# Kernel tuning notes

Hardware: AMD Instinct MI355X
Metric: run time of the kernel (lower is better)

The kernel has to match this reference:

```python
import jax, jax.numpy as jnp
import numpy as np

RANGE_DISP = 32
IND_INPUT_VIEW = np.array([1, 9]) - 1  # 0-based indices of the two input views
TOTAL_VIEWS = 9                         # an_sparse + an_novel
FEAT_CH = 64


def conv2d(x, w, b):
    # x: (N, Cin, H, W), w: (Cout, Cin, kh, kw), SAME padding, stride 1
    y = jax.lax.conv_general_dilated(x, w, (1, 1), 'SAME',
                                     dimension_numbers=('NCHW', 'OIHW', 'NCHW'))
    return y + b[None, :, None, None]


def unfold_1xK(x, K):
    # torch.nn.functional.unfold(x, kernel_size=(1, K)) for x: (M, C, H, W)
    # -> (M, C, K, H*(W-K+1)), column index = h*(W-K+1) + w (row-major).
    M, C, H, W = x.shape
    out_w = W - K + 1
    cols = jnp.arange(out_w)[None, :] + jnp.arange(K)[:, None]  # (K, out_w)
    y = x[:, :, :, cols]             # (M, C, H, K, out_w)
    y = y.transpose(0, 1, 3, 2, 4)   # (M, C, K, H, out_w)
    return y.reshape(M, C, K, H * out_w)


def setup_inputs() -> dict:
    key = jax.random.key(0)
    ks = jax.random.split(key, 24)
    b, an_sparse, an_novel, rp = 2, 2, 7, 32
    K = RANGE_DISP
    ps = rp + K - 1  # 63

    def rn(k, shape, s=1.0):
        return jax.random.normal(k, shape, dtype=jnp.float32) * s

    W = 0.05  # weight init scale
    return {
        'lf_sparse':        rn(ks[0], (b, an_sparse, rp, ps)),
        'flow_sparse':      rn(ks[1], (b, an_sparse, rp, ps)),
        'warped_lf_sparse': rn(ks[2], (b, an_sparse, rp, ps)),
        'patch_left':       rn(ks[3], (b, an_novel, rp, rp)),
        'patch_right':      rn(ks[4], (b, an_novel, rp, rp)),
        # FlowRefNet: 3 -> 64 -> 64 -> 64, 3x3 convs, SAME
        'fr_w1': rn(ks[5], (FEAT_CH, 3, 3, 3), W), 'fr_b1': jnp.zeros((FEAT_CH,), jnp.float32),
        'fr_w2': rn(ks[6], (FEAT_CH, FEAT_CH, 3, 3), W), 'fr_b2': jnp.zeros((FEAT_CH,), jnp.float32),
        'fr_w3': rn(ks[7], (FEAT_CH, FEAT_CH, 3, 3), W), 'fr_b3': jnp.zeros((FEAT_CH,), jnp.float32),
        # MlpNet: per-disparity MLP 67 -> 64 -> 64 -> 1 (weight head) + conf head 64 -> 1
        'mlp_w1': rn(ks[8], (67, 64), W), 'mlp_b1': jnp.zeros((64,), jnp.float32),
        'mlp_w2': rn(ks[9], (64, 64), W), 'mlp_b2': jnp.zeros((64,), jnp.float32),
        'mlp_w3': rn(ks[10], (64, 1), W), 'mlp_b3': jnp.zeros((1,), jnp.float32),
        'conf_w': rn(ks[11], (64, 1), W), 'conf_b': jnp.zeros((1,), jnp.float32),
        # ViewRefNet: 3 -> 64 -> 64 -> 1 convs, residual on novel patch
        'vr_w1': rn(ks[12], (FEAT_CH, 3, 3, 3), W), 'vr_b1': jnp.zeros((FEAT_CH,), jnp.float32),
        'vr_w2': rn(ks[13], (FEAT_CH, FEAT_CH, 3, 3), W), 'vr_b2': jnp.zeros((FEAT_CH,), jnp.float32),
        'vr_w3': rn(ks[14], (1, FEAT_CH, 3, 3), W), 'vr_b3': jnp.zeros((1,), jnp.float32),
    }


def reference(lf_sparse, flow_sparse, warped_lf_sparse, patch_left, patch_right,
              fr_w1, fr_b1, fr_w2, fr_b2, fr_w3, fr_b3,
              mlp_w1, mlp_b1, mlp_w2, mlp_b2, mlp_w3, mlp_b3, conf_w, conf_b,
              vr_w1, vr_b1, vr_w2, vr_b2, vr_w3, vr_b3):
    b, an_sparse, rp, ps = lf_sparse.shape
    an_novel = patch_left.shape[1]
    K = RANGE_DISP
    N = rp * rp

    lf = lf_sparse.reshape(b * an_sparse, 1, rp, ps)
    fl = flow_sparse.reshape(b * an_sparse, 1, rp, ps)
    wp = warped_lf_sparse.reshape(b * an_sparse, 1, rp, ps)

    # FlowRefNet: flow-feature extraction
    h = jax.nn.relu(conv2d(jnp.concatenate([fl, lf, wp], axis=1), fr_w1, fr_b1))
    h = jax.nn.relu(conv2d(h, fr_w2, fr_b2))
    feat = jax.nn.relu(conv2d(h, fr_w3, fr_b3))  # (b*as, 64, rp, ps)

    # angular code: input-view index minus novel-view index
    ind_novel = np.delete(np.arange(TOTAL_VIEWS), IND_INPUT_VIEW)
    ang = jnp.asarray(IND_INPUT_VIEW[None, :] - ind_novel[:, None], dtype=lf.dtype)  # (an, as)
    spatial = (jnp.arange(K) - K // 2).astype(lf.dtype)  # (K,)

    # EPI windows via unfold(kernel=(1, K))
    flow_unf = unfold_1xK(fl, K)[:, 0]  # (b*as, K, N)
    feat_unf = unfold_1xK(feat, K)      # (b*as, 64, K, N)

    sh = (b, an_novel, an_sparse)
    f_flow = jnp.broadcast_to(flow_unf.reshape(b, 1, an_sparse, 1, K, N),  sh + (1, K, N))
    f_feat = jnp.broadcast_to(feat_unf.reshape(b, 1, an_sparse, FEAT_CH, K, N), sh + (FEAT_CH, K, N))
    f_spat = jnp.broadcast_to(spatial.reshape(1, 1, 1, 1, K, 1),           sh + (1, K, N))
    f_ang  = jnp.broadcast_to(ang.reshape(1, an_novel, an_sparse, 1, 1, 1), sh + (1, K, N))
    features = jnp.concatenate([f_flow, f_feat, f_spat, f_ang], axis=3)  # (b, an, as, 67, K, N)
    # -> (b*an*as*N, K, 67) matching permute(0,3,2,1).reshape in torch
    features = features.transpose(0, 1, 2, 5, 4, 3).reshape(-1, K, 67)

    # MlpNet: per-disparity weight + per-sample confidence
    h1 = jax.nn.relu(features @ mlp_w1 + mlp_b1)
    h2 = jax.nn.relu(h1 @ mlp_w2 + mlp_b2)          # (M2, K, 64)
    weight = (h2 @ mlp_w3 + mlp_b3)[..., 0]         # (M2, K)
    conf = (h2.mean(axis=1) @ conf_w + conf_b)[..., 0]  # (M2,)

    weight = jax.nn.softmax(weight.reshape(b, an_novel, an_sparse, N, K), axis=-1)
    confs = jax.nn.softmax(conf.reshape(b, an_novel, an_sparse, N), axis=2)

    # disparity-weighted combination over EPI windows
    epi = unfold_1xK(lf, K)[:, 0].reshape(b, an_sparse, K, N)
    nv = jnp.einsum('bskn,bvsnk->bvsn', epi, weight)   # (b, an, as, N)
    novel = (nv * confs).sum(axis=2)                   # (b, an, N)

    # ViewRefNet: residual refinement
    pn = novel.reshape(b * an_novel, 1, rp, rp)
    pl = patch_left.reshape(b * an_novel, 1, rp, rp)
    pr = patch_right.reshape(b * an_novel, 1, rp, rp)
    g = jax.nn.relu(conv2d(jnp.concatenate([pn, pl, pr], axis=1), vr_w1, vr_b1))
    g = jax.nn.relu(conv2d(g, vr_w2, vr_b2))
    res = conv2d(g, vr_w3, vr_b3)
    out = pn + res
    return out.reshape(b, an_novel, rp, rp)
```

## Files before the change

kernel.cpp:

```cpp
#include <hip/hip_runtime.h>

typedef unsigned short u16;
typedef unsigned int u32;
typedef __bf16 bf16x8 __attribute__((ext_vector_type(8)));
typedef float f32x4 __attribute__((ext_vector_type(4)));
typedef u16 u16x8 __attribute__((ext_vector_type(8)));

__device__ __forceinline__ u16 f2bf(float f) {
    __bf16 h = (__bf16)f;
    return __builtin_bit_cast(u16, h);
}
__device__ __forceinline__ float bf2f(u16 u) {
    unsigned int x = ((unsigned int)u) << 16;
    return __builtin_bit_cast(float, x);
}

union FragU { u16x8 u; bf16x8 v; };

constexpr size_t X1     = 0;
constexpr size_t X2     = 258048;
constexpr size_t FEATBF = 516096;
constexpr size_t NVOFF  = 774144;
constexpr size_t CFOFF  = 802816;
constexpr size_t NOVEL  = 831488;
constexpr size_t Y1     = 845824;
constexpr size_t Y2     = 1304576;

template<int W, int NPX>
__global__ __launch_bounds__(256) void conv1_kernel(
    const float* __restrict__ in0, const float* __restrict__ in1,
    const float* __restrict__ in2,
    const float* __restrict__ wts, const float* __restrict__ bias,
    u16* __restrict__ out)
{
    constexpr int H = 32;
    const int t = threadIdx.x;
    const int px = blockIdx.y * 256 + t;
    const int m = blockIdx.z;
    const int og = blockIdx.x;
    if (px >= NPX) return;
    const int y = px / W, x = px - y * W;

    float acc[8];
#pragma unroll
    for (int oc = 0; oc < 8; ++oc) acc[oc] = bias[og * 8 + oc];

#pragma unroll
    for (int cin = 0; cin < 3; ++cin) {
        const float* ip = (cin == 0 ? in0 : (cin == 1 ? in1 : in2)) + (size_t)m * NPX;
        float tap[9];
#pragma unroll
        for (int dy = 0; dy < 3; ++dy) {
            int yy = y + dy - 1;
            bool ry = (yy >= 0) && (yy < H);
#pragma unroll
            for (int dx = 0; dx < 3; ++dx) {
                int xx = x + dx - 1;
                tap[dy * 3 + dx] = (ry && xx >= 0 && xx < W) ? ip[yy * W + xx] : 0.f;
            }
        }
#pragma unroll
        for (int oc = 0; oc < 8; ++oc) {
            const float* wr = wts + (size_t)(og * 8 + oc) * 27 + cin * 9;
#pragma unroll
            for (int j = 0; j < 9; ++j) acc[oc] = fmaf(tap[j], wr[j], acc[oc]);
        }
    }
    u16x8 pk;
#pragma unroll
    for (int oc = 0; oc < 8; ++oc) pk[oc] = f2bf(fmaxf(acc[oc], 0.f));
    *(u16x8*)(out + ((size_t)m * NPX + px) * 64 + og * 8) = pk;
}

template<int W, int NPX>
__global__ __launch_bounds__(256) void convmfma_kernel(
    const u16* __restrict__ in, const float* __restrict__ wts,
    const float* __restrict__ bias, u16* __restrict__ out)
{
    constexpr int H = 32;
    __shared__ u16 sw[5 * 64 * 64];

    const int t = threadIdx.x;
    const int base = blockIdx.x * 64;
    const int m = blockIdx.y;
    const int w = t >> 6, lane = t & 63, q = lane >> 4, l15 = lane & 15;

    const u16* im = in + (size_t)m * NPX * 64;
    const int pxA = base + w * 16 + l15;
    const int yA = pxA / W, xA = pxA - yA * W;
    const bool pxok = (pxA < NPX);

    f32x4 acc[4];
#pragma unroll
    for (int nt = 0; nt < 4; ++nt) acc[nt] = f32x4{0.f, 0.f, 0.f, 0.f};

#pragma unroll
    for (int phase = 0; phase < 2; ++phase) {
        const int tp0 = phase * 5;
        const int ntap = phase ? 4 : 5;
        if (phase) __syncthreads();
        for (int i = t; i < ntap * 4096; i += 256) {
            int tap = tp0 + (i >> 12), och = (i >> 6) & 63, cin = i & 63;
            sw[i] = f2bf(wts[(size_t)och * 576 + cin * 9 + tap]);
        }
        __syncthreads();
#pragma unroll
        for (int tl = 0; tl < 5; ++tl) {
            if (tl >= ntap) break;
            const int tap = tp0 + tl;
            const int dy = tap / 3 - 1, dx = tap % 3 - 1;
            const bool valid = pxok && (yA + dy >= 0) && (yA + dy < H)
                                    && (xA + dx >= 0) && (xA + dx < W);
            const u16* ap = im + (size_t)(pxA + dy * W + dx) * 64;
            FragU a0, a1;
            if (valid) {
                a0 = *(const FragU*)(ap + q * 8);
                a1 = *(const FragU*)(ap + 32 + q * 8);
            } else {
#pragma unroll
                for (int jj = 0; jj < 8; ++jj) { a0.u[jj] = 0; a1.u[jj] = 0; }
            }
#pragma unroll
            for (int nt = 0; nt < 4; ++nt) {
                const u16* bp = sw + tl * 4096 + (nt * 16 + l15) * 64;
                FragU b0 = *(const FragU*)(bp + q * 8);
                FragU b1 = *(const FragU*)(bp + 32 + q * 8);
                acc[nt] = __builtin_amdgcn_mfma_f32_16x16x32_bf16(a0.v, b0.v, acc[nt], 0, 0, 0);
                acc[nt] = __builtin_amdgcn_mfma_f32_16x16x32_bf16(a1.v, b1.v, acc[nt], 0, 0, 0);
            }
        }
    }

#pragma unroll
    for (int nt = 0; nt < 4; ++nt) {
        const float bb = bias[nt * 16 + l15];
#pragma unroll
        for (int e = 0; e < 4; ++e) {
            int pxs = base + w * 16 + q * 4 + e;
            if (pxs < NPX)
                out[((size_t)m * NPX + pxs) * 64 + nt * 16 + l15] =
                    f2bf(fmaxf(acc[nt][e] + bb, 0.f));
        }
    }
}

__global__ __launch_bounds__(256, 2) void mlp_mfma_kernel(
    const float* __restrict__ lf, const float* __restrict__ flow,
    const u16* __restrict__ feat,
    const float* __restrict__ w1, const float* __restrict__ b1,
    const float* __restrict__ w2, const float* __restrict__ b2,
    const float* __restrict__ w3, const float* __restrict__ b3g,
    const float* __restrict__ cw, const float* __restrict__ cbg,
    float* __restrict__ nv_out, float* __restrict__ cf_out)
{
    constexpr int SBS = 72;
    __shared__ u16 s_w1[67 * 64];
    __shared__ u16 s_w2[64 * 64];
    __shared__ __align__(16) float s_vec[7 * 64];
    __shared__ __align__(16) float s_flow[256];
    __shared__ __align__(16) float s_epi[256];
    __shared__ __align__(16) u16 s_base[256 * SBS];

    const int t = threadIdx.x;
    const int blk = blockIdx.x;
    const int bs = blk >> 7;
    const int n0 = (blk & 127) * 8;
    const int b = bs >> 1, s = bs & 1;
    const int w = t >> 6, lane = t & 63, q = lane >> 4, l15 = lane & 15;

    for (int i = t; i < 67 * 64; i += 256) s_w1[i] = f2bf(w1[i]);
    for (int i = t; i < 64 * 64; i += 256) s_w2[i] = f2bf(w2[i]);
    if (t < 64) {
        s_vec[t]       = b1[t];
        s_vec[64 + t]  = b2[t];
        s_vec[128 + t] = w3[t];
        s_vec[192 + t] = cw[t];
        s_vec[256 + t] = w1[t];
        s_vec[320 + t] = w1[65 * 64 + t];
        s_vec[384 + t] = w1[66 * 64 + t];
    }
    {
        int nl = t >> 5, k = t & 31;
        int n = n0 + nl;
        int a = (bs * 32 + (n >> 5)) * 63 + (n & 31) + k;
        s_flow[t] = flow[a];
        s_epi[t]  = lf[a];
    }
    __syncthreads();

    const float b3s = b3g[0];
    const float cbs = cbg[0];

    FragU w1b[2][4];
#pragma unroll
    for (int ks = 0; ks < 2; ++ks)
#pragma unroll
        for (int nt = 0; nt < 4; ++nt)
#pragma unroll
            for (int jj = 0; jj < 8; ++jj)
                w1b[ks][nt].u[jj] = s_w1[(1 + ks * 32 + q * 8 + jj) * 64 + nt * 16 + l15];

    float w1r0pl[4], w1r65pl[4], b1pl[4];
#pragma unroll
    for (int nt = 0; nt < 4; ++nt) {
        int j1 = nt * 16 + l15;
        w1r0pl[nt]  = s_vec[256 + j1];
        w1r65pl[nt] = s_vec[320 + j1];
        b1pl[nt]    = s_vec[j1];
    }

#pragma unroll
    for (int mt = 0; mt < 4; ++mt) {
        const int rbase = w * 64 + mt * 16;
        FragU af[2];
        {
            int r = rbase + l15;
            int n = n0 + (r >> 5);
            int pos = (n >> 5) * 63 + (n & 31) + (r & 31);
            const u16* fp = feat + ((size_t)bs * 2016 + pos) * 64;
            af[0] = *(const FragU*)(fp + q * 8);
            af[1] = *(const FragU*)(fp + 32 + q * 8);
        }
        f32x4 flow4 = *(const f32x4*)(s_flow + rbase + q * 4);
#pragma unroll
        for (int nt = 0; nt < 4; ++nt) {
            f32x4 d = {0.f, 0.f, 0.f, 0.f};
            d = __builtin_amdgcn_mfma_f32_16x16x32_bf16(af[0].v, w1b[0][nt].v, d, 0, 0, 0);
            d = __builtin_amdgcn_mfma_f32_16x16x32_bf16(af[1].v, w1b[1][nt].v, d, 0, 0, 0);
#pragma unroll
            for (int e = 0; e < 4; ++e) {
                int r = rbase + q * 4 + e;
                int k = r & 31;
                float val = d[e] + flow4[e] * w1r0pl[nt]
                          + (float)(k - 16) * w1r65pl[nt] + b1pl[nt];
                s_base[r * SBS + nt * 16 + l15] = f2bf(val);
            }
        }
    }
    __syncthreads();

    FragU w2a[4][2];
#pragma unroll
    for (int mt = 0; mt < 4; ++mt)
#pragma unroll
        for (int ks = 0; ks < 2; ++ks)
#pragma unroll
            for (int jj = 0; jj < 8; ++jj)
                w2a[mt][ks].u[jj] = s_w2[(ks * 32 + q * 8 + jj) * 64 + mt * 16 + l15];

    float w66pl[2][8];
#pragma unroll
    for (int ks = 0; ks < 2; ++ks)
#pragma unroll
        for (int jj = 0; jj < 8; ++jj)
            w66pl[ks][jj] = s_vec[384 + ks * 32 + q * 8 + jj];

    float b2pl[4][4], w3pl[4][4], cwpl[4][4];
#pragma unroll
    for (int mt = 0; mt < 4; ++mt)
#pragma unroll
        for (int e = 0; e < 4; ++e) {
            b2pl[mt][e] = s_vec[64 + mt * 16 + q * 4 + e];
            w3pl[mt][e] = s_vec[128 + mt * 16 + q * 4 + e];
            cwpl[mt][e] = s_vec[192 + mt * 16 + q * 4 + e];
        }
    float epi_pl[4];
#pragma unroll
    for (int nt = 0; nt < 4; ++nt) epi_pl[nt] = s_epi[w * 64 + nt * 16 + l15];

    for (int v = 0; v < 7; ++v) {
        float ang = (s == 0) ? -(float)(v + 1) : (float)(7 - v);
        f32x4 acc[4][4];
#pragma unroll
        for (int nt = 0; nt < 4; ++nt) {
            FragU bfr[2];
#pragma unroll
            for (int ks = 0; ks < 2; ++ks) {
                const u16x8 raw = *(const u16x8*)(s_base + (w * 64 + nt * 16 + l15) * SBS + ks * 32 + q * 8);
#pragma unroll
                for (int jj = 0; jj < 8; ++jj) {
                    float xv = bf2f(raw[jj]);
                    float hv = fmaxf(xv + ang * w66pl[ks][jj], 0.f);
                    bfr[ks].u[jj] = f2bf(hv);
                }
            }
#pragma unroll
            for (int mt = 0; mt < 4; ++mt) {
                f32x4 d = {0.f, 0.f, 0.f, 0.f};
                d = __builtin_amdgcn_mfma_f32_16x16x32_bf16(w2a[mt][0].v, bfr[0].v, d, 0, 0, 0);
                d = __builtin_amdgcn_mfma_f32_16x16x32_bf16(w2a[mt][1].v, bfr[1].v, d, 0, 0, 0);
                acc[mt][nt] = d;
            }
        }
        float wl[4], cfl[4];
#pragma unroll
        for (int nt = 0; nt < 4; ++nt) {
            float wls = 0.f, cfs = 0.f;
#pragma unroll
            for (int mt = 0; mt < 4; ++mt)
#pragma unroll
                for (int e = 0; e < 4; ++e) {
                    float h2 = fmaxf(acc[mt][nt][e] + b2pl[mt][e], 0.f);
                    wls += h2 * w3pl[mt][e];
                    cfs += h2 * cwpl[mt][e];
                }
            wls += __shfl_xor(wls, 16); wls += __shfl_xor(wls, 32);
            cfs += __shfl_xor(cfs, 16); cfs += __shfl_xor(cfs, 32);
            wl[nt]  = wls + b3s;
            cfl[nt] = cfs;
        }
#pragma unroll
        for (int ni = 0; ni < 2; ++ni) {
            float a0 = wl[ni * 2], a1 = wl[ni * 2 + 1];
            float mx = fmaxf(a0, a1);
#pragma unroll
            for (int msk = 1; msk <= 8; msk <<= 1) mx = fmaxf(mx, __shfl_xor(mx, msk));
            float e0 = __expf(a0 - mx), e1 = __expf(a1 - mx);
            float ssum = e0 + e1;
            float nvp = e0 * epi_pl[ni * 2] + e1 * epi_pl[ni * 2 + 1];
            float cfp = cfl[ni * 2] + cfl[ni * 2 + 1];
#pragma unroll
            for (int msk = 1; msk <= 8; msk <<= 1) {
                ssum += __shfl_xor(ssum, msk);
                nvp  += __shfl_xor(nvp, msk);
                cfp  += __shfl_xor(cfp, msk);
            }
            if (lane == 0) {
                int n = n0 + w * 2 + ni;
                size_t idx = ((size_t)(b * 7 + v) * 2 + s) * 1024 + n;
                nv_out[idx] = nvp / ssum;
                cf_out[idx] = cfp * (1.f / 32.f) + cbs;
            }
        }
    }
}

__global__ void combine_kernel(const float* __restrict__ nv, const float* __restrict__ cf,
                               float* __restrict__ novel) {
    int tid = blockIdx.x * 256 + threadIdx.x;
    if (tid >= 2 * 7 * 1024) return;
    int n = tid & 1023;
    int bv = tid >> 10;
    size_t i0 = ((size_t)bv * 2 + 0) * 1024 + n;
    size_t i1 = ((size_t)bv * 2 + 1) * 1024 + n;
    float c0 = cf[i0], c1 = cf[i1];
    float mx = fmaxf(c0, c1);
    float e0 = __expf(c0 - mx), e1 = __expf(c1 - mx);
    novel[tid] = (e0 * nv[i0] + e1 * nv[i1]) / (e0 + e1);
}

__global__ __launch_bounds__(256) void convlast_kernel(
    const u16* __restrict__ in,
    const float* __restrict__ wts,
    const float* __restrict__ bias,
    const float* __restrict__ resid,
    float* __restrict__ out)
{
    __shared__ float sw3[576];
    const int t = threadIdx.x;
    for (int i = t; i < 576; i += 256) sw3[i] = wts[i];
    __syncthreads();

    const int tid = blockIdx.x * 256 + t;
    const int m = tid >> 10, p = tid & 1023;
    const int y = p >> 5, x = p & 31;
    float a = bias[0] + resid[tid];
    const u16* im = in + ((size_t)m * 1024 + p) * 64;
#pragma unroll
    for (int dy = 0; dy < 3; ++dy) {
        int yy = y + dy - 1;
        if (yy < 0 || yy >= 32) continue;
#pragma unroll
        for (int dx = 0; dx < 3; ++dx) {
            int xx = x + dx - 1;
            if (xx < 0 || xx >= 32) continue;
            const u16* ip = im + (size_t)((dy - 1) * 32 + (dx - 1)) * 64;
            const int tap = dy * 3 + dx;
#pragma unroll
            for (int cg = 0; cg < 8; ++cg) {
                u16x8 raw = *(const u16x8*)(ip + cg * 8);
#pragma unroll
                for (int e = 0; e < 8; ++e)
                    a = fmaf(bf2f(raw[e]), sw3[(cg * 8 + e) * 9 + tap], a);
            }
        }
    }
    out[tid] = a;
}

extern "C" void kernel_launch(void* const* d_in, const int* in_sizes, int n_in,
                              void* d_out, int out_size, void* d_ws, size_t ws_size,
                              hipStream_t stream) {
    const float* lf   = (const float*)d_in[0];
    const float* flow = (const float*)d_in[1];
    const float* wp   = (const float*)d_in[2];
    const float* pl   = (const float*)d_in[3];
    const float* pr   = (const float*)d_in[4];
    float* ws = (float*)d_ws;

    conv1_kernel<63, 2016><<<dim3(8, 8, 4), 256, 0, stream>>>(
        flow, lf, wp, (const float*)d_in[5], (const float*)d_in[6],
        (u16*)(ws + X1));
    convmfma_kernel<63, 2016><<<dim3(32, 4), 256, 0, stream>>>(
        (const u16*)(ws + X1), (const float*)d_in[7], (const float*)d_in[8],
        (u16*)(ws + X2));
    convmfma_kernel<63, 2016><<<dim3(32, 4), 256, 0, stream>>>(
        (const u16*)(ws + X2), (const float*)d_in[9], (const float*)d_in[10],
        (u16*)(ws + FEATBF));

    mlp_mfma_kernel<<<512, 256, 0, stream>>>(
        lf, flow, (const u16*)(ws + FEATBF),
        (const float*)d_in[11], (const float*)d_in[12],
        (const float*)d_in[13], (const float*)d_in[14],
        (const float*)d_in[15], (const float*)d_in[16],
        (const float*)d_in[17], (const float*)d_in[18],
        ws + NVOFF, ws + CFOFF);

    combine_kernel<<<56, 256, 0, stream>>>(ws + NVOFF, ws + CFOFF, ws + NOVEL);

    conv1_kernel<32, 1024><<<dim3(8, 4, 14), 256, 0, stream>>>(
        ws + NOVEL, pl, pr, (const float*)d_in[19], (const float*)d_in[20],
        (u16*)(ws + Y1));
    convmfma_kernel<32, 1024><<<dim3(16, 14), 256, 0, stream>>>(
        (const u16*)(ws + Y1), (const float*)d_in[21], (const float*)d_in[22],
        (u16*)(ws + Y2));
    convlast_kernel<<<56, 256, 0, stream>>>(
        (const u16*)(ws + Y2), (const float*)d_in[23], (const float*)d_in[24],
        ws + NOVEL, (float*)d_out);
}
```

Measured before the change: 201.3 us.

## Precompute bf16 weights once, read MFMA fragments from global, fuse combine into MLP

Adds a prep kernel that converts and reorders the conv and MLP weights to bf16 once per call, so the conv and MLP kernels no longer stage and convert weights in shared memory with extra barriers. The conv kernels now load B fragments directly from global/L2. The MLP kernel is restructured so each block handles both sparse views for a batch and loops over two groups of four samples, allowing the confidence softmax combine to happen in shared memory and removing the separate combine kernel. It adds one launch and halves the MLP grid, which may lower parallelism.

```diff
diff --git a/kernel.cpp b/kernel.cpp
--- a/kernel.cpp
+++ b/kernel.cpp
@@ -17,14 +17,40 @@
 
 union FragU { u16x8 u; bf16x8 v; };
 
-constexpr size_t X1     = 0;
-constexpr size_t X2     = 258048;
-constexpr size_t FEATBF = 516096;
-constexpr size_t NVOFF  = 774144;
-constexpr size_t CFOFF  = 802816;
-constexpr size_t NOVEL  = 831488;
-constexpr size_t Y1     = 845824;
-constexpr size_t Y2     = 1304576;
+constexpr size_t WB2F  = 0;
+constexpr size_t WB3F  = 18432;
+constexpr size_t WBV2  = 36864;
+constexpr size_t W1T   = 55296;
+constexpr size_t W2T   = 57344;
+constexpr size_t X1    = 59392;
+constexpr size_t X2    = 317440;
+constexpr size_t FEATBF= 575488;
+constexpr size_t NOVEL = 833536;
+constexpr size_t Y1    = 847872;
+constexpr size_t Y2    = 1306624;
+
+__global__ __launch_bounds__(256) void prep_kernel(
+    const float* __restrict__ frw2, const float* __restrict__ frw3,
+    const float* __restrict__ vrw2,
+    const float* __restrict__ mw1, const float* __restrict__ mw2,
+    u16* __restrict__ wb2, u16* __restrict__ wb3, u16* __restrict__ wbv,
+    u16* __restrict__ w1t, u16* __restrict__ w2t)
+{
+    const int tid = blockIdx.x * 256 + threadIdx.x;
+    const int stride = gridDim.x * 256;
+    for (int i = tid; i < 36864; i += stride) {
+        int tap = i >> 12, och = (i >> 6) & 63, cin = i & 63;
+        size_t s = (size_t)och * 576 + cin * 9 + tap;
+        wb2[i] = f2bf(frw2[s]);
+        wb3[i] = f2bf(frw3[s]);
+        wbv[i] = f2bf(vrw2[s]);
+    }
+    for (int i = tid; i < 4096; i += stride) {
+        int col = i >> 6, r = i & 63;
+        w1t[i] = f2bf(mw1[(1 + r) * 64 + col]);
+        w2t[i] = f2bf(mw2[r * 64 + col]);
+    }
+}
 
 template<int W, int NPX>
 __global__ __launch_bounds__(256) void conv1_kernel(
@@ -74,12 +100,10 @@
 
 template<int W, int NPX>
 __global__ __launch_bounds__(256) void convmfma_kernel(
-    const u16* __restrict__ in, const float* __restrict__ wts,
+    const u16* __restrict__ in, const u16* __restrict__ wbf,
     const float* __restrict__ bias, u16* __restrict__ out)
 {
     constexpr int H = 32;
-    __shared__ u16 sw[5 * 64 * 64];
-
     const int t = threadIdx.x;
     const int base = blockIdx.x * 64;
     const int m = blockIdx.y;
@@ -95,39 +119,26 @@
     for (int nt = 0; nt < 4; ++nt) acc[nt] = f32x4{0.f, 0.f, 0.f, 0.f};
 
 #pragma unroll
-    for (int phase = 0; phase < 2; ++phase) {
-        const int tp0 = phase * 5;
-        const int ntap = phase ? 4 : 5;
-        if (phase) __syncthreads();
-        for (int i = t; i < ntap * 4096; i += 256) {
-            int tap = tp0 + (i >> 12), och = (i >> 6) & 63, cin = i & 63;
-            sw[i] = f2bf(wts[(size_t)och * 576 + cin * 9 + tap]);
-        }
-        __syncthreads();
-#pragma unroll
-        for (int tl = 0; tl < 5; ++tl) {
-            if (tl >= ntap) break;
-            const int tap = tp0 + tl;
-            const int dy = tap / 3 - 1, dx = tap % 3 - 1;
-            const bool valid = pxok && (yA + dy >= 0) && (yA + dy < H)
-                                    && (xA + dx >= 0) && (xA + dx < W);
-            const u16* ap = im + (size_t)(pxA + dy * W + dx) * 64;
-            FragU a0, a1;
-            if (valid) {
-                a0 = *(const FragU*)(ap + q * 8);
-                a1 = *(const FragU*)(ap + 32 + q * 8);
-            } else {
-#pragma unroll
-                for (int jj = 0; jj < 8; ++jj) { a0.u[jj] = 0; a1.u[jj] = 0; }
-            }
-#pragma unroll
-            for (int nt = 0; nt < 4; ++nt) {
-                const u16* bp = sw + tl * 4096 + (nt * 16 + l15) * 64;
-                FragU b0 = *(const FragU*)(bp + q * 8);
-                FragU b1 = *(const FragU*)(bp + 32 + q * 8);
-                acc[nt] = __builtin_amdgcn_mfma_f32_16x16x32_bf16(a0.v, b0.v, acc[nt], 0, 0, 0);
-                acc[nt] = __builtin_amdgcn_mfma_f32_16x16x32_bf16(a1.v, b1.v, acc[nt], 0, 0, 0);
-            }
+    for (int tap = 0; tap < 9; ++tap) {
+        const int dy = tap / 3 - 1, dx = tap % 3 - 1;
+        const bool valid = pxok && (yA + dy >= 0) && (yA + dy < H)
+                                && (xA + dx >= 0) && (xA + dx < W);
+        const u16* ap = im + (size_t)(pxA + dy * W + dx) * 64;
+        FragU a0, a1;
+        if (valid) {
+            a0 = *(const FragU*)(ap + q * 8);
+            a1 = *(const FragU*)(ap + 32 + q * 8);
+        } else {
+#pragma unroll
+            for (int jj = 0; jj < 8; ++jj) { a0.u[jj] = 0; a1.u[jj] = 0; }
+        }
+#pragma unroll
+        for (int nt = 0; nt < 4; ++nt) {
+            const u16* bp = wbf + tap * 4096 + (nt * 16 + l15) * 64;
+            FragU b0 = *(const FragU*)(bp + q * 8);
+            FragU b1 = *(const FragU*)(bp + 32 + q * 8);
+            acc[nt] = __builtin_amdgcn_mfma_f32_16x16x32_bf16(a0.v, b0.v, acc[nt], 0, 0, 0);
+            acc[nt] = __builtin_amdgcn_mfma_f32_16x16x32_bf16(a1.v, b1.v, acc[nt], 0, 0, 0);
         }
     }
 
@@ -147,29 +158,29 @@
 __global__ __launch_bounds__(256, 2) void mlp_mfma_kernel(
     const float* __restrict__ lf, const float* __restrict__ flow,
     const u16* __restrict__ feat,
+    const u16* __restrict__ w1t, const u16* __restrict__ w2t,
     const float* __restrict__ w1, const float* __restrict__ b1,
-    const float* __restrict__ w2, const float* __restrict__ b2,
+    const float* __restrict__ b2,
     const float* __restrict__ w3, const float* __restrict__ b3g,
     const float* __restrict__ cw, const float* __restrict__ cbg,
-    float* __restrict__ nv_out, float* __restrict__ cf_out)
+    float* __restrict__ novel)
 {
     constexpr int SBS = 72;
-    __shared__ u16 s_w1[67 * 64];
-    __shared__ u16 s_w2[64 * 64];
     __shared__ __align__(16) float s_vec[7 * 64];
     __shared__ __align__(16) float s_flow[256];
     __shared__ __align__(16) float s_epi[256];
     __shared__ __align__(16) u16 s_base[256 * SBS];
+    __shared__ float s_nv[2][7][4];
+    __shared__ float s_cf[2][7][4];
 
     const int t = threadIdx.x;
     const int blk = blockIdx.x;
-    const int bs = blk >> 7;
-    const int n0 = (blk & 127) * 8;
-    const int b = bs >> 1, s = bs & 1;
+    const int b = blk >> 7;
+    const int n0base = (blk & 127) * 8;
     const int w = t >> 6, lane = t & 63, q = lane >> 4, l15 = lane & 15;
-
-    for (int i = t; i < 67 * 64; i += 256) s_w1[i] = f2bf(w1[i]);
-    for (int i = t; i < 64 * 64; i += 256) s_w2[i] = f2bf(w2[i]);
+    const int sw = w >> 1;
+    const int bsw = b * 2 + sw;
+
     if (t < 64) {
         s_vec[t]       = b1[t];
         s_vec[64 + t]  = b2[t];
@@ -179,13 +190,6 @@
         s_vec[320 + t] = w1[65 * 64 + t];
         s_vec[384 + t] = w1[66 * 64 + t];
     }
-    {
-        int nl = t >> 5, k = t & 31;
-        int n = n0 + nl;
-        int a = (bs * 32 + (n >> 5)) * 63 + (n & 31) + k;
-        s_flow[t] = flow[a];
-        s_epi[t]  = lf[a];
-    }
     __syncthreads();
 
     const float b3s = b3g[0];
@@ -196,9 +200,14 @@
     for (int ks = 0; ks < 2; ++ks)
 #pragma unroll
         for (int nt = 0; nt < 4; ++nt)
-#pragma unroll
-            for (int jj = 0; jj < 8; ++jj)
-                w1b[ks][nt].u[jj] = s_w1[(1 + ks * 32 + q * 8 + jj) * 64 + nt * 16 + l15];
+            w1b[ks][nt] = *(const FragU*)(w1t + (nt * 16 + l15) * 64 + ks * 32 + q * 8);
+
+    FragU w2a[4][2];
+#pragma unroll
+    for (int mt = 0; mt < 4; ++mt)
+#pragma unroll
+        for (int ks = 0; ks < 2; ++ks)
+            w2a[mt][ks] = *(const FragU*)(w2t + (mt * 16 + l15) * 64 + ks * 32 + q * 8);
 
     float w1r0pl[4], w1r65pl[4], b1pl[4];
 #pragma unroll
@@ -208,53 +217,12 @@
         w1r65pl[nt] = s_vec[320 + j1];
         b1pl[nt]    = s_vec[j1];
     }
-
-#pragma unroll
-    for (int mt = 0; mt < 4; ++mt) {
-        const int rbase = w * 64 + mt * 16;
-        FragU af[2];
-        {
-            int r = rbase + l15;
-            int n = n0 + (r >> 5);
-            int pos = (n >> 5) * 63 + (n & 31) + (r & 31);
-            const u16* fp = feat + ((size_t)bs * 2016 + pos) * 64;
-            af[0] = *(const FragU*)(fp + q * 8);
-            af[1] = *(const FragU*)(fp + 32 + q * 8);
-        }
-        f32x4 flow4 = *(const f32x4*)(s_flow + rbase + q * 4);
-#pragma unroll
-        for (int nt = 0; nt < 4; ++nt) {
-            f32x4 d = {0.f, 0.f, 0.f, 0.f};
-            d = __builtin_amdgcn_mfma_f32_16x16x32_bf16(af[0].v, w1b[0][nt].v, d, 0, 0, 0);
-            d = __builtin_amdgcn_mfma_f32_16x16x32_bf16(af[1].v, w1b[1][nt].v, d, 0, 0, 0);
-#pragma unroll
-            for (int e = 0; e < 4; ++e) {
-                int r = rbase + q * 4 + e;
-                int k = r & 31;
-                float val = d[e] + flow4[e] * w1r0pl[nt]
-                          + (float)(k - 16) * w1r65pl[nt] + b1pl[nt];
-                s_base[r * SBS + nt * 16 + l15] = f2bf(val);
-            }
-        }
-    }
-    __syncthreads();
-
-    FragU w2a[4][2];
-#pragma unroll
-    for (int mt = 0; mt < 4; ++mt)
-#pragma unroll
-        for (int ks = 0; ks < 2; ++ks)
-#pragma unroll
-            for (int jj = 0; jj < 8; ++jj)
-                w2a[mt][ks].u[jj] = s_w2[(ks * 32 + q * 8 + jj) * 64 + mt * 16 + l15];
-
     float w66pl[2][8];
 #pragma unroll
     for (int ks = 0; ks < 2; ++ks)
 #pragma unroll
         for (int jj = 0; jj < 8; ++jj)
             w66pl[ks][jj] = s_vec[384 + ks * 32 + q * 8 + jj];
-
     float b2pl[4][4], w3pl[4][4], cwpl[4][4];
 #pragma unroll
     for (int mt = 0; mt < 4; ++mt)
@@ -264,89 +232,128 @@
             w3pl[mt][e] = s_vec[128 + mt * 16 + q * 4 + e];
             cwpl[mt][e] = s_vec[192 + mt * 16 + q * 4 + e];
         }
-    float epi_pl[4];
-#pragma unroll
-    for (int nt = 0; nt < 4; ++nt) epi_pl[nt] = s_epi[w * 64 + nt * 16 + l15];
-
-    for (int v = 0; v < 7; ++v) {
-        float ang = (s == 0) ? -(float)(v + 1) : (float)(7 - v);
-        f32x4 acc[4][4];
-#pragma unroll
-        for (int nt = 0; nt < 4; ++nt) {
-            FragU bfr[2];
-#pragma unroll
-            for (int ks = 0; ks < 2; ++ks) {
-                const u16x8 raw = *(const u16x8*)(s_base + (w * 64 + nt * 16 + l15) * SBS + ks * 32 + q * 8);
-#pragma unroll
-                for (int jj = 0; jj < 8; ++jj) {
-                    float xv = bf2f(raw[jj]);
-                    float hv = fmaxf(xv + ang * w66pl[ks][jj], 0.f);
-                    bfr[ks].u[jj] = f2bf(hv);
+
+#pragma unroll 1
+    for (int iter = 0; iter < 2; ++iter) {
+        const int n0 = n0base + iter * 4;
+        {
+            int ss = t >> 7, nl = (t >> 5) & 3, k = t & 31;
+            int n = n0 + nl;
+            int a = ((b * 2 + ss) * 32 + (n >> 5)) * 63 + (n & 31) + k;
+            s_flow[t] = flow[a];
+            s_epi[t]  = lf[a];
+        }
+        __syncthreads();
+
+#pragma unroll
+        for (int mt = 0; mt < 4; ++mt) {
+            const int rbase = w * 64 + mt * 16;
+            FragU af[2];
+            {
+                int r = rbase + l15;
+                int n = n0 + ((r >> 5) & 3);
+                int pos = (n >> 5) * 63 + (n & 31) + (r & 31);
+                const u16* fp = feat + ((size_t)bsw * 2016 + pos) * 64;
+                af[0] = *(const FragU*)(fp + q * 8);
+                af[1] = *(const FragU*)(fp + 32 + q * 8);
+            }
+            f32x4 flow4 = *(const f32x4*)(s_flow + rbase + q * 4);
+#pragma unroll
+            for (int nt = 0; nt < 4; ++nt) {
+                f32x4 d = {0.f, 0.f, 0.f, 0.f};
+                d = __builtin_amdgcn_mfma_f32_16x16x32_bf16(af[0].v, w1b[0][nt].v, d, 0, 0, 0);
+                d = __builtin_amdgcn_mfma_f32_16x16x32_bf16(af[1].v, w1b[1][nt].v, d, 0, 0, 0);
+#pragma unroll
+                for (int e = 0; e < 4; ++e) {
+                    int r = rbase + q * 4 + e;
+                    int k = r & 31;
+                    float val = d[e] + flow4[e] * w1r0pl[nt]
+                              + (float)(k - 16) * w1r65pl[nt] + b1pl[nt];
+                    s_base[r * SBS + nt * 16 + l15] = f2bf(val);
                 }
             }
-#pragma unroll
-            for (int mt = 0; mt < 4; ++mt) {
-                f32x4 d = {0.f, 0.f, 0.f, 0.f};
-                d = __builtin_amdgcn_mfma_f32_16x16x32_bf16(w2a[mt][0].v, bfr[0].v, d, 0, 0, 0);
-                d = __builtin_amdgcn_mfma_f32_16x16x32_bf16(w2a[mt][1].v, bfr[1].v, d, 0, 0, 0);
-                acc[mt][nt] = d;
-            }
-        }
-        float wl[4], cfl[4];
-#pragma unroll
-        for (int nt = 0; nt < 4; ++nt) {
-            float wls = 0.f, cfs = 0.f;
-#pragma unroll
-            for (int mt = 0; mt < 4; ++mt)
-#pragma unroll
-                for (int e = 0; e < 4; ++e) {
-                    float h2 = fmaxf(acc[mt][nt][e] + b2pl[mt][e], 0.f);
-                    wls += h2 * w3pl[mt][e];
-                    cfs += h2 * cwpl[mt][e];
+        }
+        __syncthreads();
+
+        float epi_pl[4];
+#pragma unroll
+        for (int nt = 0; nt < 4; ++nt) epi_pl[nt] = s_epi[w * 64 + nt * 16 + l15];
+
+        for (int v = 0; v < 7; ++v) {
+            float ang = (sw == 0) ? -(float)(v + 1) : (float)(7 - v);
+            f32x4 acc[4][4];
+#pragma unroll
+            for (int nt = 0; nt < 4; ++nt) {
+                FragU bfr[2];
+#pragma unroll
+                for (int ks = 0; ks < 2; ++ks) {
+                    const u16x8 raw = *(const u16x8*)(s_base + (w * 64 + nt * 16 + l15) * SBS + ks * 32 + q * 8);
+#pragma unroll
+                    for (int jj = 0; jj < 8; ++jj) {
+                        float xv = bf2f(raw[jj]);
+                        float hv = fmaxf(xv + ang * w66pl[ks][jj], 0.f);
+                        bfr[ks].u[jj] = f2bf(hv);
+                    }
                 }
-            wls += __shfl_xor(wls, 16); wls += __shfl_xor(wls, 32);
-            cfs += __shfl_xor(cfs, 16); cfs += __shfl_xor(cfs, 32);
-            wl[nt]  = wls + b3s;
-            cfl[nt] = cfs;
-        }
-#pragma unroll
-        for (int ni = 0; ni < 2; ++ni) {
-            float a0 = wl[ni * 2], a1 = wl[ni * 2 + 1];
-            float mx = fmaxf(a0, a1);
-#pragma unroll
-            for (int msk = 1; msk <= 8; msk <<= 1) mx = fmaxf(mx, __shfl_xor(mx, msk));
-            float e0 = __expf(a0 - mx), e1 = __expf(a1 - mx);
-            float ssum = e0 + e1;
-            float nvp = e0 * epi_pl[ni * 2] + e1 * epi_pl[ni * 2 + 1];
-            float cfp = cfl[ni * 2] + cfl[ni * 2 + 1];
-#pragma unroll
-            for (int msk = 1; msk <= 8; msk <<= 1) {
-                ssum += __shfl_xor(ssum, msk);
-                nvp  += __shfl_xor(nvp, msk);
-                cfp  += __shfl_xor(cfp, msk);
-            }
-            if (lane == 0) {
-                int n = n0 + w * 2 + ni;
-                size_t idx = ((size_t)(b * 7 + v) * 2 + s) * 1024 + n;
-                nv_out[idx] = nvp / ssum;
-                cf_out[idx] = cfp * (1.f / 32.f) + cbs;
-            }
-        }
-    }
-}
-
-__global__ void combine_kernel(const float* __restrict__ nv, const float* __restrict__ cf,
-                               float* __restrict__ novel) {
-    int tid = blockIdx.x * 256 + threadIdx.x;
-    if (tid >= 2 * 7 * 1024) return;
-    int n = tid & 1023;
-    int bv = tid >> 10;
-    size_t i0 = ((size_t)bv * 2 + 0) * 1024 + n;
-    size_t i1 = ((size_t)bv * 2 + 1) * 1024 + n;
-    float c0 = cf[i0], c1 = cf[i1];
-    float mx = fmaxf(c0, c1);
-    float e0 = __expf(c0 - mx), e1 = __expf(c1 - mx);
-    novel[tid] = (e0 * nv[i0] + e1 * nv[i1]) / (e0 + e1);
+#pragma unroll
+                for (int mt = 0; mt < 4; ++mt) {
+                    f32x4 d = {0.f, 0.f, 0.f, 0.f};
+                    d = __builtin_amdgcn_mfma_f32_16x16x32_bf16(w2a[mt][0].v, bfr[0].v, d, 0, 0, 0);
+                    d = __builtin_amdgcn_mfma_f32_16x16x32_bf16(w2a[mt][1].v, bfr[1].v, d, 0, 0, 0);
+                    acc[mt][nt] = d;
+                }
+            }
+            float wl[4], cfl[4];
+#pragma unroll
+            for (int nt = 0; nt < 4; ++nt) {
+                float wls = 0.f, cfs = 0.f;
+#pragma unroll
+                for (int mt = 0; mt < 4; ++mt)
+#pragma unroll
+                    for (int e = 0; e < 4; ++e) {
+                        float h2 = fmaxf(acc[mt][nt][e] + b2pl[mt][e], 0.f);
+                        wls += h2 * w3pl[mt][e];
+                        cfs += h2 * cwpl[mt][e];
+                    }
+                wls += __shfl_xor(wls, 16); wls += __shfl_xor(wls, 32);
+                cfs += __shfl_xor(cfs, 16); cfs += __shfl_xor(cfs, 32);
+                wl[nt]  = wls + b3s;
+                cfl[nt] = cfs;
+            }
+#pragma unroll
+            for (int ni = 0; ni < 2; ++ni) {
+                float a0 = wl[ni * 2], a1 = wl[ni * 2 + 1];
+                float mx = fmaxf(a0, a1);
+#pragma unroll
+                for (int msk = 1; msk <= 8; msk <<= 1) mx = fmaxf(mx, __shfl_xor(mx, msk));
+                float e0 = __expf(a0 - mx), e1 = __expf(a1 - mx);
+                float ssum = e0 + e1;
+                float nvp = e0 * epi_pl[ni * 2] + e1 * epi_pl[ni * 2 + 1];
+                float cfp = cfl[ni * 2] + cfl[ni * 2 + 1];
+#pragma unroll
+                for (int msk = 1; msk <= 8; msk <<= 1) {
+                    ssum += __shfl_xor(ssum, msk);
+                    nvp  += __shfl_xor(nvp, msk);
+                    cfp  += __shfl_xor(cfp, msk);
+                }
+                if (lane == 0) {
+                    int nloc = (w & 1) * 2 + ni;
+                    s_nv[sw][v][nloc] = nvp / ssum;
+                    s_cf[sw][v][nloc] = cfp * (1.f / 32.f) + cbs;
+                }
+            }
+        }
+        __syncthreads();
+
+        if (t < 28) {
+            int v = t >> 2, nl = t & 3;
+            float c0 = s_cf[0][v][nl], c1 = s_cf[1][v][nl];
+            float mx = fmaxf(c0, c1);
+            float e0 = __expf(c0 - mx), e1 = __expf(c1 - mx);
+            novel[(size_t)(b * 7 + v) * 1024 + n0 + nl] =
+                (e0 * s_nv[0][v][nl] + e1 * s_nv[1][v][nl]) / (e0 + e1);
+        }
+    }
 }
 
 __global__ __launch_bounds__(256) void convlast_kernel(
@@ -398,31 +405,36 @@
     const float* pr   = (const float*)d_in[4];
     float* ws = (float*)d_ws;
 
+    prep_kernel<<<128, 256, 0, stream>>>(
+        (const float*)d_in[7], (const float*)d_in[9], (const float*)d_in[21],
+        (const float*)d_in[11], (const float*)d_in[13],
+        (u16*)(ws + WB2F), (u16*)(ws + WB3F), (u16*)(ws + WBV2),
+        (u16*)(ws + W1T), (u16*)(ws + W2T));
+
     conv1_kernel<63, 2016><<<dim3(8, 8, 4), 256, 0, stream>>>(
         flow, lf, wp, (const float*)d_in[5], (const float*)d_in[6],
         (u16*)(ws + X1));
     convmfma_kernel<63, 2016><<<dim3(32, 4), 256, 0, stream>>>(
-        (const u16*)(ws + X1), (const float*)d_in[7], (const float*)d_in[8],
+        (const u16*)(ws + X1), (const u16*)(ws + WB2F), (const float*)d_in[8],
         (u16*)(ws + X2));
     convmfma_kernel<63, 2016><<<dim3(32, 4), 256, 0, stream>>>(
-        (const u16*)(ws + X2), (const float*)d_in[9], (const float*)d_in[10],
+        (const u16*)(ws + X2), (const u16*)(ws + WB3F), (const float*)d_in[10],
         (u16*)(ws + FEATBF));
 
-    mlp_mfma_kernel<<<512, 256, 0, stream>>>(
+    mlp_mfma_kernel<<<256, 256, 0, stream>>>(
         lf, flow, (const u16*)(ws + FEATBF),
+        (const u16*)(ws + W1T), (const u16*)(ws + W2T),
         (const float*)d_in[11], (const float*)d_in[12],
-        (const float*)d_in[13], (const float*)d_in[14],
+        (const float*)d_in[14],
         (const float*)d_in[15], (const float*)d_in[16],
         (const float*)d_in[17], (const float*)d_in[18],
-        ws + NVOFF, ws + CFOFF);
-
-    combine_kernel<<<56, 256, 0, stream>>>(ws + NVOFF, ws + CFOFF, ws + NOVEL);
+        ws + NOVEL);
 
     conv1_kernel<32, 1024><<<dim3(8, 4, 14), 256, 0, stream>>>(
         ws + NOVEL, pl, pr, (const float*)d_in[19], (const float*)d_in[20],
         (u16*)(ws + Y1));
     convmfma_kernel<32, 1024><<<dim3(16, 14), 256, 0, stream>>>(
-        (const u16*)(ws + Y1), (const float*)d_in[21], (const float*)d_in[22],
+        (const u16*)(ws + Y1), (const u16*)(ws + WBV2), (const float*)d_in[22],
         (u16*)(ws + Y2));
     convlast_kernel<<<56, 256, 0, stream>>>(
         (const u16*)(ws + Y2), (const float*)d_in[23], (const float*)d_in[24],
```

Result: slower. 218.5 us (+8.5%).
